# Kernel tuning notes

Measured on AMD Instinct MI355X. Metric: run time of the kernel, lower is better.

The kernel has to match this reference:

```python
import jax, jax.numpy as jnp
import numpy as np
import math

B, S, H = 2, 2048, 2048
NQ, NKV, HD = 16, 4, 128
THETA = 10000.0


def rotate_half(x):
    x1, x2 = jnp.split(x, 2, axis=-1)
    return jnp.concatenate([-x2, x1], axis=-1)


def rope_cos_sin(position_ids, dim, base, dtype):
    # inv_freq: (dim/2,)
    inv_freq = 1.0 / (base ** (jnp.arange(0, dim, 2, dtype=jnp.float32) / dim))
    freqs = position_ids.astype(jnp.float32)[..., None] * inv_freq  # (B, S, dim/2)
    emb = jnp.concatenate([freqs, freqs], axis=-1)  # (B, S, dim)
    return jnp.cos(emb).astype(dtype), jnp.sin(emb).astype(dtype)


def setup_inputs() -> dict:
    key = jax.random.key(0)
    ks = jax.random.split(key, 5)
    hidden_states = jax.random.normal(ks[0], (B, S, H), dtype=jnp.float32)
    position_ids = jnp.broadcast_to(jnp.arange(S, dtype=jnp.int32)[None, :], (B, S))
    sc = 0.02
    wq = jax.random.normal(ks[1], (NQ * HD, H), dtype=jnp.float32) * sc
    wk = jax.random.normal(ks[2], (NKV * HD, H), dtype=jnp.float32) * sc
    wv = jax.random.normal(ks[3], (NKV * HD, H), dtype=jnp.float32) * sc
    wo = jax.random.normal(ks[4], (H, NQ * HD), dtype=jnp.float32) * sc
    return {"hidden_states": hidden_states, "position_ids": position_ids,
            "wq": wq, "wk": wk, "wv": wv, "wo": wo}


def reference(hidden_states, position_ids, wq, wk, wv, wo):
    b, s, _ = hidden_states.shape
    n_rep = NQ // NKV
    # QKV projections (no bias)
    q = (hidden_states @ wq.T).reshape(b, s, NQ, HD).transpose(0, 2, 1, 3)   # (b, nq, s, hd)
    k = (hidden_states @ wk.T).reshape(b, s, NKV, HD).transpose(0, 2, 1, 3)  # (b, nkv, s, hd)
    v = (hidden_states @ wv.T).reshape(b, s, NKV, HD).transpose(0, 2, 1, 3)
    # RoPE (full rotary, partial_rotary_factor == 1.0)
    cos, sin = rope_cos_sin(position_ids, HD, THETA, q.dtype)  # (b, s, hd)
    cos = cos[:, None, :, :]
    sin = sin[:, None, :, :]
    q = q * cos + rotate_half(q) * sin
    k = k * cos + rotate_half(k) * sin
    # repeat_kv for GQA: (b, nkv, s, hd) -> (b, nq, s, hd)
    k = jnp.repeat(k, n_rep, axis=1)
    v = jnp.repeat(v, n_rep, axis=1)
    # scores (b, nq, s, s)
    scores = jnp.einsum('bhqd,bhkd->bhqk', q, k) / math.sqrt(HD)
    causal = jnp.triu(jnp.full((s, s), -jnp.inf, dtype=scores.dtype), k=1)
    scores = scores + causal
    probs = jax.nn.softmax(scores.astype(jnp.float32), axis=-1).astype(q.dtype)
    out = jnp.einsum('bhqk,bhkd->bhqd', probs, v)  # (b, nq, s, hd)
    out = out.transpose(0, 2, 1, 3).reshape(b, s, NQ * HD)
    return out @ wo.T
```

## Files before the change

### kernel.cpp

```cpp
#include <hip/hip_runtime.h>
#include <hip/hip_bf16.h>
#include <cstdint>

typedef unsigned short u16;
typedef __attribute__((ext_vector_type(4))) float f32x4;
typedef __attribute__((ext_vector_type(8))) short s16x8;
typedef __attribute__((ext_vector_type(4))) unsigned int u32x4;
typedef __attribute__((ext_vector_type(2))) unsigned int u32x2;
typedef __attribute__((ext_vector_type(4))) unsigned short u16x4;
typedef __attribute__((ext_vector_type(8))) unsigned short u16x8;

#define MFMA16(a, b, c) __builtin_amdgcn_mfma_f32_16x16x32_bf16(a, b, c, 0, 0, 0)
#define GLOAD16(g, l) __builtin_amdgcn_global_load_lds((const __attribute__((address_space(1))) void*)(g), (__attribute__((address_space(3))) void*)(l), 16, 0, 0)

__device__ __forceinline__ u16 f2bf(float f) {
    union { float f; uint32_t u; } v{f};
    uint32_t r = v.u + 0x7FFF + ((v.u >> 16) & 1);
    return (u16)(r >> 16);
}
__device__ __forceinline__ float bf2f(u16 b) {
    union { uint32_t u; float f; } v;
    v.u = ((uint32_t)b) << 16;
    return v.f;
}

__global__ void cast_f32_bf16(const float* __restrict__ in, u16* __restrict__ out, int n4) {
    int i = blockIdx.x * 256 + threadIdx.x;
    if (i >= n4) return;
    float4 f = ((const float4*)in)[i];
    u16x4 o = { f2bf(f.x), f2bf(f.y), f2bf(f.z), f2bf(f.w) };
    ((u16x4*)out)[i] = o;
}

__global__ void rope_table_k(const int* __restrict__ pos, float* __restrict__ ct, float* __restrict__ st) {
    int i = blockIdx.x * 256 + threadIdx.x;
    int j = i & 63;
    int bs = i >> 6;
    float p = (float)pos[bs];
    float invf = powf(10000.0f, -(float)j * (1.0f / 64.0f));
    float ang = p * invf;
    ct[i] = cosf(ang);
    st[i] = sinf(ang);
}

template <int FUSE>
__global__ __launch_bounds__(256) void gemm_bt(const u16* __restrict__ A, const u16* __restrict__ Bw,
                                               float* __restrict__ C, int M, int N, int K,
                                               const float* __restrict__ ct, const float* __restrict__ st,
                                               u16* __restrict__ Qb, u16* __restrict__ Kb,
                                               u16* __restrict__ Vb) {
    __shared__ u16 Sh[32768];
    const int tid = threadIdx.x;
    const int lane = tid & 63, wid = tid >> 6;
    const int g = lane >> 4, r = lane & 15;

    const int gx = gridDim.x, nwg = gx * gridDim.y;
    int lid = blockIdx.y * gx + blockIdx.x;
    int swz = (lid % 8) * (nwg / 8) + lid / 8;
    const int bxi = swz % gx, byi = swz / gx;

    const size_t bm = (size_t)byi * 128, bn = (size_t)bxi * 128;
    const int wr = (wid >> 1) * 64, wc = (wid & 1) * 64;

    const int srow = wid * 32 + (lane >> 3);
    const int schunk = (lane & 7) ^ ((lane >> 3) & 7);
    const u16* aSrc = A + (bm + srow) * (size_t)K + schunk * 8;
    const u16* bSrc = Bw + (bn + srow) * (size_t)K + schunk * 8;

    auto STAGE = [&](int ktEl, int bi) {
        u16* aD = Sh + bi * 16384 + wid * 2048;
        u16* bD = Sh + bi * 16384 + 8192 + wid * 2048;
#pragma unroll
        for (int j = 0; j < 4; ++j) {
            GLOAD16(aSrc + (size_t)(j * 8) * K + ktEl, aD + j * 512);
            GLOAD16(bSrc + (size_t)(j * 8) * K + ktEl, bD + j * 512);
        }
    };

    f32x4 acc[4][4] = {};
    const int nk = K >> 6;
    STAGE(0, 0);
    __syncthreads();
    for (int t = 0; t < nk; ++t) {
        if (t + 1 < nk) STAGE((t + 1) << 6, (t + 1) & 1);
        const u16* As = Sh + (t & 1) * 16384;
        const u16* Bs = As + 8192;
        s16x8 af[4][2], bfr[4][2];
#pragma unroll
        for (int m = 0; m < 4; ++m)
#pragma unroll
            for (int kk = 0; kk < 2; ++kk) {
                int rowa = wr + m * 16 + r;
                af[m][kk] = *(const s16x8*)(As + rowa * 64 + (((kk * 4 + g) ^ (rowa & 7)) << 3));
                int rowb = wc + m * 16 + r;
                bfr[m][kk] = *(const s16x8*)(Bs + rowb * 64 + (((kk * 4 + g) ^ (rowb & 7)) << 3));
            }
#pragma unroll
        for (int m = 0; m < 4; ++m)
#pragma unroll
            for (int n = 0; n < 4; ++n) {
                acc[m][n] = MFMA16(af[m][0], bfr[n][0], acc[m][n]);
                acc[m][n] = MFMA16(af[m][1], bfr[n][1], acc[m][n]);
            }
        __syncthreads();
    }
    if (FUSE == 0) {
#pragma unroll
        for (int m = 0; m < 4; ++m)
#pragma unroll
            for (int n = 0; n < 4; ++n)
#pragma unroll
                for (int i = 0; i < 4; ++i) {
                    size_t row = bm + wr + m * 16 + g * 4 + i;
                    size_t col = bn + wc + n * 16 + r;
                    C[row * N + col] = acc[m][n][i];
                }
        return;
    }
    const int hb = bxi;
    if (hb < 20) {
#pragma unroll
        for (int m = 0; m < 4; ++m)
#pragma unroll
            for (int n = 0; n < 4; ++n)
#pragma unroll
                for (int i = 0; i < 4; ++i) {
                    int rowl = wr + m * 16 + g * 4 + i;
                    int col = wc + n * 16 + r;
                    int c4 = col >> 3;
                    *(u16*)((char*)Sh + rowl * 256 + (((c4 ^ (rowl & 15))) << 4) + ((col & 7) << 1)) =
                        f2bf(acc[m][n][i]);
                }
        __syncthreads();
        if (tid < 128) {
            const int rowl = tid;
            const size_t tok = bm + rowl;
            const int b = (int)(tok >> 11), s = (int)(tok & 2047);
            u16* dst;
            if (hb < 16) dst = Qb + (((size_t)(b * 16 + hb) * 2048 + s) << 7);
            else         dst = Kb + (((size_t)(b * 4 + (hb - 16)) * 2048 + s) << 7);
            const char* tb = (const char*)Sh + rowl * 256;
            const float* ctr = ct + tok * 64;
            const float* str = st + tok * 64;
#pragma unroll
            for (int c4 = 0; c4 < 8; ++c4) {
                u32x4 lo4 = *(const u32x4*)(tb + ((c4 ^ (rowl & 15)) << 4));
                u32x4 hi4 = *(const u32x4*)(tb + (((c4 + 8) ^ (rowl & 15)) << 4));
                const u16* lo = (const u16*)&lo4;
                const u16* hi = (const u16*)&hi4;
                u16x4 o0, o1, o2, o3;
                u16* olo[2] = { (u16*)&o0, (u16*)&o1 };
                u16* ohi[2] = { (u16*)&o2, (u16*)&o3 };
#pragma unroll
                for (int j = 0; j < 8; ++j) {
                    float c = ctr[c4 * 8 + j], sn = str[c4 * 8 + j];
                    float xl = bf2f(lo[j]), xh = bf2f(hi[j]);
                    olo[j >> 2][j & 3] = f2bf(xl * c - xh * sn);
                    ohi[j >> 2][j & 3] = f2bf(xh * c + xl * sn);
                }
                *(u16x4*)(dst + c4 * 8) = o0;
                *(u16x4*)(dst + c4 * 8 + 4) = o1;
                *(u16x4*)(dst + 64 + c4 * 8) = o2;
                *(u16x4*)(dst + 64 + c4 * 8 + 4) = o3;
            }
        }
    } else {
#pragma unroll
        for (int m = 0; m < 4; ++m) {
            int tokb = wr + m * 16 + g * 4;
            int chunk = tokb >> 3;
            int sub = (g & 1) * 8;
#pragma unroll
            for (int n = 0; n < 4; ++n) {
                int d = wc + n * 16 + r;
                u16x4 v = { f2bf(acc[m][n][0]), f2bf(acc[m][n][1]),
                            f2bf(acc[m][n][2]), f2bf(acc[m][n][3]) };
                *(u16x4*)((char*)Sh + d * 256 + (((chunk ^ (d & 15))) << 4) + sub) = v;
            }
        }
        __syncthreads();
        const int b = (int)(bm >> 11), s0 = (int)(bm & 2047);
        u16* dst = Vb + (size_t)(b * 4 + (hb - 20)) * 262144;
        const int dd = tid >> 1, half = (tid & 1) * 8;
#pragma unroll
        for (int c8 = 0; c8 < 8; ++c8) {
            int sc = half + c8;
            u32x4 v4 = *(const u32x4*)((const char*)Sh + dd * 256 + (((sc ^ (dd & 15))) << 4));
            *(u32x4*)(dst + (size_t)dd * 2048 + s0 + sc * 8) = v4;
        }
    }
}

__global__ __launch_bounds__(256, 2) void attn_k(const u16* __restrict__ Qb, const u16* __restrict__ Kb,
                                                 const u16* __restrict__ Vb, u16* __restrict__ Ob) {
    __shared__ char smem[49152];
    u16* Ksh = (u16*)smem;
    u16* Vts = (u16*)(smem + 16384);
    char* Pall = smem + 32768;
    const int tid = threadIdx.x;
    const int lane = tid & 63, w = tid >> 6;
    const int g = lane >> 4, r = lane & 15;

    const int lid = blockIdx.y * gridDim.x + blockIdx.x;
    const int cpy = lid >> 8, p = lid & 255;
    const int bh = p & 31;
    const int qblk = cpy ? (7 - (p >> 5)) : ((p >> 5) + 8);

    const int b = bh >> 4, h = bh & 15;
    const int hkv = h >> 2;
    const int q0 = qblk * 128;
    const u16* Qh = Qb + ((size_t)(b * 16 + h) << 18);
    const u16* Kh = Kb + ((size_t)(b * 4 + hkv) << 18);
    const u16* Vh = Vb + ((size_t)(b * 4 + hkv) << 18);

    s16x8 qf[2][4];
#pragma unroll
    for (int qq = 0; qq < 2; ++qq)
#pragma unroll
        for (int c = 0; c < 4; ++c)
            qf[qq][c] = *(const s16x8*)(Qh + (size_t)(q0 + qq * 64 + w * 16 + r) * 128 + c * 32 + g * 8);

    f32x4 o[2][8] = {};
    float mrun[2] = {-1e30f, -1e30f};
    float lrun[2] = {0.f, 0.f};
    const int fmax[2] = { q0 + w * 16 + 15, q0 + 64 + w * 16 + 15 };

    const int ntiles = 2 * qblk + 2;
    const int krow0 = tid >> 4, kch = tid & 15;

    u32x4 kpr[4], vpr[4];
#pragma unroll
    for (int it = 0; it < 4; ++it)
        kpr[it] = *(const u32x4*)(Kh + (size_t)(krow0 + it * 16) * 128 + kch * 8);
#pragma unroll
    for (int it = 0; it < 4; ++it) {
        int task = tid + it * 256;
        vpr[it] = *(const u32x4*)(Vh + (size_t)(task >> 3) * 2048 + (task & 7) * 8);
    }

    for (int t = 0; t < ntiles; ++t) {
        const int kv0 = t * 64;
        __syncthreads();
#pragma unroll
        for (int it = 0; it < 4; ++it) {
            int row = krow0 + it * 16;
            *(u32x4*)((char*)Ksh + row * 256 + ((kch ^ (row & 7)) << 4)) = kpr[it];
        }
#pragma unroll
        for (int it = 0; it < 4; ++it) {
            int task = tid + it * 256;
            int d = task >> 3, ch = task & 7;
            *(u32x4*)((char*)Vts + d * 128 + ((ch ^ (d & 7) ^ ((d >> 3) & 7)) << 4)) = vpr[it];
        }
        __syncthreads();
        if (t + 1 < ntiles) {
            const int kn = kv0 + 64;
#pragma unroll
            for (int it = 0; it < 4; ++it)
                kpr[it] = *(const u32x4*)(Kh + (size_t)(kn + krow0 + it * 16) * 128 + kch * 8);
#pragma unroll
            for (int it = 0; it < 4; ++it) {
                int task = tid + it * 256;
                vpr[it] = *(const u32x4*)(Vh + (size_t)(task >> 3) * 2048 + kn + (task & 7) * 8);
            }
        }
        f32x4 st4[2][4];
#pragma unroll
        for (int ts = 0; ts < 4; ++ts) {
            int row = ts * 16 + r;
            s16x8 kf[4];
#pragma unroll
            for (int c = 0; c < 4; ++c)
                kf[c] = *(const s16x8*)((const char*)Ksh + row * 256 + (((c * 4 + g) ^ (row & 7)) << 4));
            f32x4 a0 = {}, a1 = {};
            if (kv0 <= fmax[0])
#pragma unroll
                for (int c = 0; c < 4; ++c) a0 = MFMA16(kf[c], qf[0][c], a0);
            if (kv0 <= fmax[1])
#pragma unroll
                for (int c = 0; c < 4; ++c) a1 = MFMA16(kf[c], qf[1][c], a1);
            st4[0][ts] = a0;
            st4[1][ts] = a1;
        }
#pragma unroll
        for (int qq = 0; qq < 2; ++qq) {
            if (kv0 > fmax[qq]) continue;
            const int qg = q0 + qq * 64 + w * 16 + r;
            float sv[16];
            float mtile = -1e30f;
#pragma unroll
            for (int ts = 0; ts < 4; ++ts)
#pragma unroll
                for (int i = 0; i < 4; ++i) {
                    int kvg = kv0 + ts * 16 + g * 4 + i;
                    float s = st4[qq][ts][i] * 0.08838834764831845f;
                    s = (kvg > qg) ? -1e30f : s;
                    sv[ts * 4 + i] = s;
                    mtile = fmaxf(mtile, s);
                }
            mtile = fmaxf(mtile, __shfl_xor(mtile, 16));
            mtile = fmaxf(mtile, __shfl_xor(mtile, 32));
            float mnew = fmaxf(mrun[qq], mtile);
            float corr = __expf(mrun[qq] - mnew);
            float psum = 0.f;
            unsigned int pw[8];
#pragma unroll
            for (int ts = 0; ts < 4; ++ts) {
                float p0 = __expf(sv[ts * 4 + 0] - mnew);
                float p1 = __expf(sv[ts * 4 + 1] - mnew);
                float p2 = __expf(sv[ts * 4 + 2] - mnew);
                float p3 = __expf(sv[ts * 4 + 3] - mnew);
                psum += (p0 + p1) + (p2 + p3);
                pw[ts * 2 + 0] = (unsigned int)f2bf(p0) | ((unsigned int)f2bf(p1) << 16);
                pw[ts * 2 + 1] = (unsigned int)f2bf(p2) | ((unsigned int)f2bf(p3) << 16);
            }
            psum += __shfl_xor(psum, 16);
            psum += __shfl_xor(psum, 32);
            lrun[qq] = lrun[qq] * corr + psum;
            mrun[qq] = mnew;
#pragma unroll
            for (int dsb = 0; dsb < 8; ++dsb)
#pragma unroll
                for (int i = 0; i < 4; ++i) o[qq][dsb][i] *= corr;
            char* pbase = Pall + (w * 2 + qq) * 2048;
#pragma unroll
            for (int ts = 0; ts < 4; ++ts) {
                int chunk = (ts * 2 + (g >> 1)) ^ (r & 7);
                u32x2 val = { pw[ts * 2], pw[ts * 2 + 1] };
                *(u32x2*)(pbase + r * 128 + chunk * 16 + (g & 1) * 8) = val;
            }
        }
        asm volatile("s_waitcnt lgkmcnt(0)" ::: "memory");
#pragma unroll
        for (int c = 0; c < 2; ++c) {
            s16x8 vf[8];
#pragma unroll
            for (int dsb = 0; dsb < 8; ++dsb) {
                int d = dsb * 16 + r;
                vf[dsb] = *(const s16x8*)((const char*)Vts + d * 128 +
                    ((((c * 4 + g) ^ (d & 7) ^ ((d >> 3) & 7))) << 4));
            }
#pragma unroll
            for (int qq = 0; qq < 2; ++qq) {
                if (kv0 > fmax[qq]) continue;
                s16x8 pf = *(const s16x8*)(Pall + (w * 2 + qq) * 2048 + r * 128 +
                                           (((c * 4 + g) ^ (r & 7)) << 4));
#pragma unroll
                for (int dsb = 0; dsb < 8; ++dsb)
                    o[qq][dsb] = MFMA16(vf[dsb], pf, o[qq][dsb]);
            }
        }
    }
    __syncthreads();
#pragma unroll
    for (int qq = 0; qq < 2; ++qq) {
        float linv = 1.0f / lrun[qq];
        char* obase = smem + (w << 13) + (qq << 12);
#pragma unroll
        for (int dsb = 0; dsb < 8; ++dsb)
#pragma unroll
            for (int i = 0; i < 4; ++i) {
                int d = dsb * 16 + g * 4 + i;
                *(u16*)(obase + r * 256 + d * 2) = f2bf(o[qq][dsb][i] * linv);
            }
    }
    asm volatile("s_waitcnt lgkmcnt(0)" ::: "memory");
    const int rr = lane >> 2, cbo = (lane & 3) * 32;
#pragma unroll
    for (int qq = 0; qq < 2; ++qq) {
        char* obase = smem + (w << 13) + (qq << 12);
        size_t oidx = ((size_t)b * 2048 + q0 + qq * 64 + w * 16 + rr) * 2048 + h * 128 + cbo;
#pragma unroll
        for (int p2 = 0; p2 < 4; ++p2) {
            u32x4 vv = *(const u32x4*)(obase + rr * 256 + cbo * 2 + p2 * 16);
            *(u32x4*)(Ob + oidx + p2 * 8) = vv;
        }
    }
}

extern "C" void kernel_launch(void* const* d_in, const int* in_sizes, int n_in,
                              void* d_out, int out_size, void* d_ws, size_t ws_size,
                              hipStream_t stream) {
    const float* hidden = (const float*)d_in[0];
    const int* pos = (const int*)d_in[1];
    const float* wq = (const float*)d_in[2];
    const float* wk = (const float*)d_in[3];
    const float* wv = (const float*)d_in[4];
    const float* wo = (const float*)d_in[5];
    float* out = (float*)d_out;

    char* ws = (char*)d_ws;
    size_t off = 0;
    auto alloc = [&](size_t bytes) { char* p = ws + off; off += (bytes + 255) & ~255ULL; return p; };
    u16* Xb   = (u16*)alloc(8388608ULL * 2);
    u16* WB   = (u16*)alloc(6291456ULL * 2);
    u16* WoB  = (u16*)alloc(4194304ULL * 2);
    u16* Qb   = (u16*)alloc(8388608ULL * 2);
    u16* Kb   = (u16*)alloc(2097152ULL * 2);
    u16* Vb   = (u16*)alloc(2097152ULL * 2);
    u16* Ab   = (u16*)alloc(8388608ULL * 2);
    float* ctab = (float*)alloc(262144ULL * 4);
    float* stab = (float*)alloc(262144ULL * 4);

    cast_f32_bf16<<<8192, 256, 0, stream>>>(hidden, Xb, 2097152);
    cast_f32_bf16<<<4096, 256, 0, stream>>>(wq, WB, 1048576);
    cast_f32_bf16<<<1024, 256, 0, stream>>>(wk, WB + 4194304, 262144);
    cast_f32_bf16<<<1024, 256, 0, stream>>>(wv, WB + 5242880, 262144);
    cast_f32_bf16<<<4096, 256, 0, stream>>>(wo, WoB, 1048576);
    rope_table_k<<<1024, 256, 0, stream>>>(pos, ctab, stab);
    gemm_bt<1><<<dim3(24, 32), 256, 0, stream>>>(Xb, WB, nullptr, 4096, 3072, 2048,
                                                 ctab, stab, Qb, Kb, Vb);
    attn_k<<<dim3(16, 32), 256, 0, stream>>>(Qb, Kb, Vb, Ab);
    gemm_bt<0><<<dim3(16, 32), 256, 0, stream>>>(Ab, WoB, out, 4096, 2048, 2048,
                                                 nullptr, nullptr, nullptr, nullptr, nullptr);
}
```

Baseline: 241.6 us.

## Fuse casts into one launch, defer rescale in softmax, move prefetch before barrier

The five f32-to-bf16 cast launches become a single kernel that picks its source and destination by index range, cutting launch overhead. In attention, the online-softmax rescale of the output accumulators is skipped while the tile max stays within 8 of the running max (a lazy rescale), which removes the exp and many multiplies on most tiles. The global prefetch of the next K/V tile is issued before the barrier instead of after it. The lazy rescale lets unnormalized exponentials grow up to e^8 before rescaling, which relies on float range and slightly changes the bf16 rounding of P.

```diff
diff --git a/kernel.cpp b/kernel.cpp
--- a/kernel.cpp
+++ b/kernel.cpp
@@ -24,12 +24,20 @@
     return v.f;
 }
 
-__global__ void cast_f32_bf16(const float* __restrict__ in, u16* __restrict__ out, int n4) {
+__global__ void cast_all(const float* __restrict__ h, const float* __restrict__ wq,
+                         const float* __restrict__ wk, const float* __restrict__ wv,
+                         const float* __restrict__ wo, u16* __restrict__ Xb,
+                         u16* __restrict__ WB, u16* __restrict__ WoB) {
     int i = blockIdx.x * 256 + threadIdx.x;
-    if (i >= n4) return;
-    float4 f = ((const float4*)in)[i];
+    const float* src; u16* dst; int off;
+    if (i < 2097152)      { src = h;  dst = Xb;           off = i; }
+    else if (i < 3145728) { src = wq; dst = WB;           off = i - 2097152; }
+    else if (i < 3407872) { src = wk; dst = WB + 4194304; off = i - 3145728; }
+    else if (i < 3670016) { src = wv; dst = WB + 5242880; off = i - 3407872; }
+    else                  { src = wo; dst = WoB;          off = i - 3670016; }
+    float4 f = ((const float4*)src)[off];
     u16x4 o = { f2bf(f.x), f2bf(f.y), f2bf(f.z), f2bf(f.w) };
-    ((u16x4*)out)[i] = o;
+    ((u16x4*)dst)[off] = o;
 }
 
 __global__ void rope_table_k(const int* __restrict__ pos, float* __restrict__ ct, float* __restrict__ st) {
@@ -252,7 +260,6 @@
             int d = task >> 3, ch = task & 7;
             *(u32x4*)((char*)Vts + d * 128 + ((ch ^ (d & 7) ^ ((d >> 3) & 7)) << 4)) = vpr[it];
         }
-        __syncthreads();
         if (t + 1 < ntiles) {
             const int kn = kv0 + 64;
 #pragma unroll
@@ -264,6 +271,7 @@
                 vpr[it] = *(const u32x4*)(Vh + (size_t)(task >> 3) * 2048 + kn + (task & 7) * 8);
             }
         }
+        __syncthreads();
         f32x4 st4[2][4];
 #pragma unroll
         for (int ts = 0; ts < 4; ++ts) {
@@ -300,28 +308,33 @@
                 }
             mtile = fmaxf(mtile, __shfl_xor(mtile, 16));
             mtile = fmaxf(mtile, __shfl_xor(mtile, 32));
-            float mnew = fmaxf(mrun[qq], mtile);
-            float corr = __expf(mrun[qq] - mnew);
+            float mold = mrun[qq];
+            if (!__all(mtile <= mold + 8.0f)) {
+                float mnew = fmaxf(mold, mtile);
+                float corr = __expf(mold - mnew);
+#pragma unroll
+                for (int dsb = 0; dsb < 8; ++dsb)
+#pragma unroll
+                    for (int i = 0; i < 4; ++i) o[qq][dsb][i] *= corr;
+                lrun[qq] *= corr;
+                mrun[qq] = mnew;
+            }
+            float mm = mrun[qq];
             float psum = 0.f;
             unsigned int pw[8];
 #pragma unroll
             for (int ts = 0; ts < 4; ++ts) {
-                float p0 = __expf(sv[ts * 4 + 0] - mnew);
-                float p1 = __expf(sv[ts * 4 + 1] - mnew);
-                float p2 = __expf(sv[ts * 4 + 2] - mnew);
-                float p3 = __expf(sv[ts * 4 + 3] - mnew);
+                float p0 = __expf(sv[ts * 4 + 0] - mm);
+                float p1 = __expf(sv[ts * 4 + 1] - mm);
+                float p2 = __expf(sv[ts * 4 + 2] - mm);
+                float p3 = __expf(sv[ts * 4 + 3] - mm);
                 psum += (p0 + p1) + (p2 + p3);
                 pw[ts * 2 + 0] = (unsigned int)f2bf(p0) | ((unsigned int)f2bf(p1) << 16);
                 pw[ts * 2 + 1] = (unsigned int)f2bf(p2) | ((unsigned int)f2bf(p3) << 16);
             }
             psum += __shfl_xor(psum, 16);
             psum += __shfl_xor(psum, 32);
-            lrun[qq] = lrun[qq] * corr + psum;
-            mrun[qq] = mnew;
-#pragma unroll
-            for (int dsb = 0; dsb < 8; ++dsb)
-#pragma unroll
-                for (int i = 0; i < 4; ++i) o[qq][dsb][i] *= corr;
+            lrun[qq] += psum;
             char* pbase = Pall + (w * 2 + qq) * 2048;
 #pragma unroll
             for (int ts = 0; ts < 4; ++ts) {
@@ -402,11 +415,7 @@
     float* ctab = (float*)alloc(262144ULL * 4);
     float* stab = (float*)alloc(262144ULL * 4);
 
-    cast_f32_bf16<<<8192, 256, 0, stream>>>(hidden, Xb, 2097152);
-    cast_f32_bf16<<<4096, 256, 0, stream>>>(wq, WB, 1048576);
-    cast_f32_bf16<<<1024, 256, 0, stream>>>(wk, WB + 4194304, 262144);
-    cast_f32_bf16<<<1024, 256, 0, stream>>>(wv, WB + 5242880, 262144);
-    cast_f32_bf16<<<4096, 256, 0, stream>>>(wo, WoB, 1048576);
+    cast_all<<<18432, 256, 0, stream>>>(hidden, wq, wk, wv, wo, Xb, WB, WoB);
     rope_table_k<<<1024, 256, 0, stream>>>(pos, ctab, stab);
     gemm_bt<1><<<dim3(24, 32), 256, 0, stream>>>(Xb, WB, nullptr, 4096, 3072, 2048,
                                                  ctab, stab, Qb, Kb, Vb);
```

New measurement: 234.2 us. -3.0%, faster.
